# Performance work log

Measured on AMD Instinct MI355X. Metric: run time of the kernel, lower is better.

Reference implementation:

```python
import jax, jax.numpy as jnp
import numpy as np
import math

D_MODEL = 1024
N_HEADS = 16
D_HEAD = D_MODEL // N_HEADS
D_FF = 4096
BOTTLENECK = D_MODEL // 4  # 256
AB_HIDDEN = max(D_MODEL // 32, 8)  # 32
EPS = 1e-6


def rms_norm(x, w):
    rms = jnp.sqrt(jnp.mean(x * x, axis=-1, keepdims=True) + EPS)
    return x / rms * w


def rotate_half(x):
    x1, x2 = jnp.split(x, 2, axis=-1)
    return jnp.concatenate([-x2, x1], axis=-1)


def rope_tables(T, dim):
    inv_freq = 1.0 / (10000.0 ** (jnp.arange(0, dim, 2, dtype=jnp.float32) / dim))
    t = jnp.arange(T, dtype=jnp.float32)
    freqs = jnp.outer(t, inv_freq)            # [T, dim/2]
    emb = jnp.concatenate([freqs, freqs], -1)  # [T, dim]
    return jnp.cos(emb), jnp.sin(emb)


def setup_inputs() -> dict:
    key = jax.random.key(0)
    ks = jax.random.split(key, 12)
    B, T = 4, 2048
    s = lambda fan_in: 1.0 / math.sqrt(fan_in)
    x = jax.random.normal(ks[0], (B, T, D_MODEL), jnp.float32)
    mask = jnp.tril(jnp.ones((T, T), jnp.int32))  # causal 0/1 mask, mask==0 -> -inf
    return {
        "x": x,
        "mask": mask,
        "norm1_w": jnp.ones((D_MODEL,), jnp.float32),
        "Wq": jax.random.normal(ks[1], (D_MODEL, D_MODEL), jnp.float32) * s(D_MODEL),
        "Wk": jax.random.normal(ks[2], (D_MODEL, D_MODEL), jnp.float32) * s(D_MODEL),
        "Wv": jax.random.normal(ks[3], (D_MODEL, D_MODEL), jnp.float32) * s(D_MODEL),
        "Wo": jax.random.normal(ks[4], (D_MODEL, D_MODEL), jnp.float32) * s(D_MODEL),
        "norm2_w": jnp.ones((D_MODEL,), jnp.float32),
        "w1": jax.random.normal(ks[5], (D_FF, D_MODEL), jnp.float32) * s(D_MODEL),
        "w2": jax.random.normal(ks[6], (D_MODEL, D_FF), jnp.float32) * s(D_FF),
        "fc1": jax.random.normal(ks[7], (AB_HIDDEN, D_MODEL), jnp.float32) * s(D_MODEL),
        "fc2": jax.random.normal(ks[8], (2, AB_HIDDEN), jnp.float32) * s(AB_HIDDEN),
        "down": jax.random.normal(ks[9], (BOTTLENECK, D_MODEL), jnp.float32) * s(D_MODEL),
        "up": jax.random.normal(ks[10], (D_MODEL, BOTTLENECK), jnp.float32) * s(BOTTLENECK),
    }


def attention(x, mask, Wq, Wk, Wv, Wo):
    B, T, D = x.shape
    def split_heads(y):
        return y.reshape(B, T, N_HEADS, D_HEAD).transpose(0, 2, 1, 3)  # [B,H,T,Dh]
    q = split_heads(x @ Wq.T)
    k = split_heads(x @ Wk.T)
    v = split_heads(x @ Wv.T)
    cos, sin = rope_tables(T, D_HEAD)
    cos = cos[None, None]; sin = sin[None, None]
    q = q * cos + rotate_half(q) * sin
    k = k * cos + rotate_half(k) * sin
    scores = jnp.einsum("bhqd,bhkd->bhqk", q, k) / math.sqrt(D_HEAD)
    scores = jnp.where(mask[:T, :T] == 0, -jnp.inf, scores)
    attn = jax.nn.softmax(scores, axis=-1)
    out = jnp.einsum("bhqk,bhkd->bhqd", attn, v)
    out = out.transpose(0, 2, 1, 3).reshape(B, T, D)
    return out @ Wo.T


def reference(x, mask, norm1_w, Wq, Wk, Wv, Wo, norm2_w, w1, w2, fc1, fc2, down, up):
    # group='B': gated FFN + projection branch (dropout=0 / eval mode)
    x = x + attention(rms_norm(x, norm1_w), mask, Wq, Wk, Wv, Wo)
    normed = rms_norm(x, norm2_w)
    ffn_out = jax.nn.gelu(normed @ w1.T, approximate=False) @ w2.T
    # AttentionAlphaBetaLM: mean over tokens, tiny MLP -> (alpha, beta)
    g = normed.mean(axis=1)                      # [B, D]
    h = jax.nn.relu(g @ fc1.T)                   # [B, hidden]
    ab = h @ fc2.T                               # [B, 2]
    alpha = jax.nn.sigmoid(ab[:, 0])             # [B]
    beta = jax.nn.sigmoid(ab[:, 1])              # allow_negative_beta=False for group B
    proj_out = jax.nn.relu(normed @ down.T) @ up.T
    x = x + alpha[:, None, None] * ffn_out + beta[:, None, None] * proj_out
    return x
```

## Files before the change

kernel.cpp:

```cpp
#include <hip/hip_runtime.h>
#include <hip/hip_bf16.h>
#include <math.h>

typedef unsigned short u16;
typedef unsigned int   u32;

typedef __bf16 bf16x8_t __attribute__((ext_vector_type(8)));
typedef float  f32x4_t  __attribute__((ext_vector_type(4)));

__device__ float AB_dev[8];

__device__ inline float bf2f(u16 u) {
    u32 x = ((u32)u) << 16;
    return __builtin_bit_cast(float, x);
}
__device__ inline u16 f2bf(float f) {
    u32 x = __builtin_bit_cast(u32, f);
    return (u16)((x + 0x7fffu + ((x >> 16) & 1u)) >> 16);
}
__device__ inline u32 cvt_pk_bf16(float lo, float hi) {
    u32 r;
    asm("v_cvt_pk_bf16_f32 %0, %1, %2" : "=v"(r) : "v"(lo), "v"(hi));
    return r;
}
__device__ inline uint4 stage_pack_f32(const float* p) {
    float4 f0 = ((const float4*)p)[0];
    float4 f1 = ((const float4*)p)[1];
    u32 w0 = (u32)f2bf(f0.x) | ((u32)f2bf(f0.y) << 16);
    u32 w1 = (u32)f2bf(f0.z) | ((u32)f2bf(f0.w) << 16);
    u32 w2 = (u32)f2bf(f1.x) | ((u32)f2bf(f1.y) << 16);
    u32 w3 = (u32)f2bf(f1.z) | ((u32)f2bf(f1.w) << 16);
    return uint4{w0, w1, w2, w3};
}
#define GLD(gptr, lptr) __builtin_amdgcn_global_load_lds( \
    (const __attribute__((address_space(1))) void*)(gptr), \
    (__attribute__((address_space(3))) void*)(lptr), 16, 0, 0)

template <typename TIN>
__global__ __launch_bounds__(256) void rmsnorm_kernel(
    const TIN* __restrict__ x, const float* __restrict__ w, u16* __restrict__ out)
{
    const int row = blockIdx.x, tid = threadIdx.x;
    const size_t rb = (size_t)row * 1024;
    float val[4];
#pragma unroll
    for (int i = 0; i < 4; ++i) {
        size_t idx = rb + tid + i * 256;
        if constexpr (sizeof(TIN) == 4) val[i] = ((const float*)x)[idx];
        else                            val[i] = bf2f(((const u16*)x)[idx]);
    }
    float ss = val[0]*val[0] + val[1]*val[1] + val[2]*val[2] + val[3]*val[3];
#pragma unroll
    for (int off = 32; off >= 1; off >>= 1) ss += __shfl_xor(ss, off, 64);
    __shared__ float red[4];
    if ((tid & 63) == 0) red[tid >> 6] = ss;
    __syncthreads();
    float tot = red[0] + red[1] + red[2] + red[3];
    float inv = rsqrtf(tot * (1.0f / 1024.0f) + 1e-6f);
    u16* orow = out + rb;
#pragma unroll
    for (int i = 0; i < 4; ++i)
        orow[tid + i * 256] = f2bf(val[i] * inv * w[tid + i * 256]);
}

__global__ __launch_bounds__(256) void convm_kernel(
    const float* __restrict__ s0, const float* __restrict__ s1,
    const float* __restrict__ s2, const float* __restrict__ s3,
    u16* __restrict__ d0, u16* __restrict__ d1,
    u16* __restrict__ d2, u16* __restrict__ d3, int shift)
{
    int sel = blockIdx.x >> shift;
    int loc = blockIdx.x & ((1 << shift) - 1);
    const float* s = sel == 0 ? s0 : sel == 1 ? s1 : sel == 2 ? s2 : s3;
    u16*       d = sel == 0 ? d0 : sel == 1 ? d1 : sel == 2 ? d2 : d3;
    size_t i = ((size_t)loc * 256 + threadIdx.x) * 8;
    *(uint4*)(d + i) = stage_pack_f32(s + i);
}

enum { EPI_QKV = 0, EPI_ADDX_F32 = 1, EPI_GELU = 2, EPI_COMB0 = 3,
       EPI_COMBA = 4, EPI_RELU = 5, EPI_BSCALE = 6 };

__device__ inline void xcd_remap(int& bx, int& by) {
    int nwg = gridDim.x * gridDim.y;
    int bid = blockIdx.y * gridDim.x + blockIdx.x;
    int q8 = nwg >> 3;
    int swz = (bid & 7) * q8 + (bid >> 3);
    bx = swz % gridDim.x;
    by = swz / gridDim.x;
}

template <int EPI>
__global__ __launch_bounds__(256) void gemm128e(
    const u16* __restrict__ A, int sA, const u16* __restrict__ Wb, int sW,
    void* __restrict__ C, const float* __restrict__ Xf,
    const u16* __restrict__ Xh, int N, int K)
{
    __shared__ __align__(16) u16 As[2][128 * 32];
    __shared__ __align__(16) u16 Bs[2][128 * 32];
    const int tid  = threadIdx.x;
    const int wave = tid >> 6, lane = tid & 63;
    const int quad = lane >> 4, l16 = lane & 15;
    int bxx, byy;
    xcd_remap(bxx, byy);
    const int row0 = byy * 128, col0 = bxx * 128;
    const int wm = (wave >> 1) * 64, wn = (wave & 1) * 64;

    f32x4_t acc[4][4];
#pragma unroll
    for (int i = 0; i < 4; ++i)
#pragma unroll
        for (int j = 0; j < 4; ++j) { f32x4_t z = {0,0,0,0}; acc[i][j] = z; }

    const u16* Abase = A + (size_t)row0 * sA;
    const int id0 = tid, id1 = tid + 256;
    const size_t aoff0 = (size_t)(id0 >> 2) * sA + (id0 & 3) * 8;
    const size_t aoff1 = (size_t)(id1 >> 2) * sA + (id1 & 3) * 8;
    const size_t boff0 = (size_t)(col0 + (id0 >> 2)) * sW + (id0 & 3) * 8;
    const size_t boff1 = (size_t)(col0 + (id1 >> 2)) * sW + (id1 & 3) * 8;
    const size_t ld0 = (size_t)(wave * 64) * 8;
    const size_t ld1 = (size_t)(256 + wave * 64) * 8;

    for (int k0 = 0; k0 < K; k0 += 64) {
        __syncthreads();
        GLD(Abase + aoff0 + k0,      As[0] + ld0);
        GLD(Abase + aoff1 + k0,      As[0] + ld1);
        GLD(Abase + aoff0 + k0 + 32, As[1] + ld0);
        GLD(Abase + aoff1 + k0 + 32, As[1] + ld1);
        GLD(Wb + boff0 + k0,         Bs[0] + ld0);
        GLD(Wb + boff1 + k0,         Bs[0] + ld1);
        GLD(Wb + boff0 + k0 + 32,    Bs[1] + ld0);
        GLD(Wb + boff1 + k0 + 32,    Bs[1] + ld1);
        __syncthreads();

#pragma unroll
        for (int hh = 0; hh < 2; ++hh) {
            const bf16x8_t* As8 = (const bf16x8_t*)As[hh];
            const bf16x8_t* Bs8 = (const bf16x8_t*)Bs[hh];
            bf16x8_t af[4], bfr[4];
#pragma unroll
            for (int i = 0; i < 4; ++i) {
                af[i]  = As8[(wm + i * 16 + l16) * 4 + quad];
                bfr[i] = Bs8[(wn + i * 16 + l16) * 4 + quad];
            }
#pragma unroll
            for (int i = 0; i < 4; ++i)
#pragma unroll
                for (int j = 0; j < 4; ++j)
                    acc[i][j] = __builtin_amdgcn_mfma_f32_16x16x32_bf16(
                        af[i], bfr[j], acc[i][j], 0, 0, 0);
        }
    }

    float al = 0.0f;
    if (EPI == EPI_COMB0 || EPI == EPI_COMBA)
        al = AB_dev[byy >> 4];
#pragma unroll
    for (int i = 0; i < 4; ++i) {
        int mbase = row0 + wm + i * 16 + quad * 4;
#pragma unroll
        for (int j = 0; j < 4; ++j) {
            int n = col0 + wn + j * 16 + l16;
#pragma unroll
            for (int r = 0; r < 4; ++r) {
                float vv = acc[i][j][r];
                int row = mbase + r;
                if (EPI == EPI_QKV) {
                    int sel = col0 >> 10;
                    float sc = (sel == 0) ? 0.18033688011112042f : 1.0f;
                    ((u16*)C)[(size_t)sel * 8388608 + (size_t)row * 1024 + (n & 1023)]
                        = f2bf(vv * sc);
                } else if (EPI == EPI_ADDX_F32) {
                    size_t off = (size_t)row * N + n;
                    ((u16*)C)[off] = f2bf(vv + Xf[off]);
                } else if (EPI == EPI_GELU) {
                    size_t off = (size_t)row * N + n;
                    vv = 0.5f * vv * (1.0f + erff(vv * 0.70710678118654752f));
                    ((u16*)C)[off] = f2bf(vv);
                } else {
                    size_t off = (size_t)row * N + n;
                    float prev = ((float*)C)[off];
                    float add = (EPI == EPI_COMB0) ? bf2f(Xh[off]) : 0.0f;
                    ((float*)C)[off] = prev + add + al * vv;
                }
            }
        }
    }
}

template <int EPI>
__global__ __launch_bounds__(256) void gemm64b(
    const u16* __restrict__ A, int sA, const u16* __restrict__ Wb, int sW,
    void* __restrict__ C, int N, int K)
{
    __shared__ __align__(16) u16 As[2][128 * 32];
    __shared__ __align__(16) u16 Bs[2][64 * 32];
    const int tid  = threadIdx.x;
    const int wave = tid >> 6, lane = tid & 63;
    const int quad = lane >> 4, l16 = lane & 15;
    int bxx, byy;
    xcd_remap(bxx, byy);
    const int row0 = byy * 128, col0 = bxx * 64;
    const int wm = (wave >> 1) * 64, wn = (wave & 1) * 32;

    f32x4_t acc[4][2];
#pragma unroll
    for (int i = 0; i < 4; ++i)
#pragma unroll
        for (int j = 0; j < 2; ++j) { f32x4_t z = {0,0,0,0}; acc[i][j] = z; }

    const u16* Abase = A + (size_t)row0 * sA;
    const int id0 = tid, id1 = tid + 256;
    const size_t aoff0 = (size_t)(id0 >> 2) * sA + (id0 & 3) * 8;
    const size_t aoff1 = (size_t)(id1 >> 2) * sA + (id1 & 3) * 8;
    const size_t woff  = (size_t)(col0 + (tid >> 2)) * sW + (tid & 3) * 8;
    const size_t ld0 = (size_t)(wave * 64) * 8;
    const size_t ld1 = (size_t)(256 + wave * 64) * 8;

    for (int k0 = 0; k0 < K; k0 += 64) {
        __syncthreads();
        GLD(Abase + aoff0 + k0,      As[0] + ld0);
        GLD(Abase + aoff1 + k0,      As[0] + ld1);
        GLD(Abase + aoff0 + k0 + 32, As[1] + ld0);
        GLD(Abase + aoff1 + k0 + 32, As[1] + ld1);
        GLD(Wb + woff + k0,          Bs[0] + ld0);
        GLD(Wb + woff + k0 + 32,     Bs[1] + ld0);
        __syncthreads();

#pragma unroll
        for (int hh = 0; hh < 2; ++hh) {
            const bf16x8_t* As8 = (const bf16x8_t*)As[hh];
            const bf16x8_t* Bs8 = (const bf16x8_t*)Bs[hh];
            bf16x8_t af[4], bfr[2];
#pragma unroll
            for (int i = 0; i < 4; ++i) af[i]  = As8[(wm + i * 16 + l16) * 4 + quad];
#pragma unroll
            for (int j = 0; j < 2; ++j) bfr[j] = Bs8[(wn + j * 16 + l16) * 4 + quad];
#pragma unroll
            for (int i = 0; i < 4; ++i)
#pragma unroll
                for (int j = 0; j < 2; ++j)
                    acc[i][j] = __builtin_amdgcn_mfma_f32_16x16x32_bf16(
                        af[i], bfr[j], acc[i][j], 0, 0, 0);
        }
    }

#pragma unroll
    for (int i = 0; i < 4; ++i) {
        int mbase = row0 + wm + i * 16 + quad * 4;
#pragma unroll
        for (int j = 0; j < 2; ++j) {
            int n = col0 + wn + j * 16 + l16;
#pragma unroll
            for (int r = 0; r < 4; ++r) {
                float vv = acc[i][j][r];
                int row = mbase + r;
                size_t off = (size_t)row * N + n;
                if (EPI == EPI_RELU) {
                    ((u16*)C)[off] = f2bf(fmaxf(vv, 0.0f));
                } else {
                    ((float*)C)[off] = AB_dev[4 + (row >> 11)] * vv;
                }
            }
        }
    }
}

__global__ __launch_bounds__(256) void rope_kernel(u16* __restrict__ q, u16* __restrict__ k)
{
    int idx = blockIdx.x * 256 + threadIdx.x;
    int i = idx & 31;
    int h = (idx >> 5) & 15;
    int t = (idx >> 9) & 2047;
    int b = idx >> 20;
    float inv = __expf(-(float)i * (9.210340371976184f / 32.0f));
    float ang = (float)t * inv;
    float sn, cs;
    sincosf(ang, &sn, &cs);
    size_t o1 = ((size_t)(b * 2048 + t)) * 1024 + h * 64 + i;
    size_t o2 = o1 + 32;
    float q1 = bf2f(q[o1]), q2 = bf2f(q[o2]);
    q[o1] = f2bf(q1 * cs - q2 * sn);
    q[o2] = f2bf(q2 * cs + q1 * sn);
    float k1 = bf2f(k[o1]), k2 = bf2f(k[o2]);
    k[o1] = f2bf(k1 * cs - k2 * sn);
    k[o2] = f2bf(k2 * cs + k1 * sn);
}

#define TS 72

__global__ __launch_bounds__(256) void flash_kernel(
    const u16* __restrict__ q, const u16* __restrict__ k,
    const u16* __restrict__ v, u16* __restrict__ o)
{
    __shared__ __align__(16) u16 QP[128 * TS];
    __shared__ __align__(16) u16 KT[2][64 * 64];
    __shared__ __align__(16) u16 VT[64 * TS];

    const int tid  = threadIdx.x;
    const int wave = tid >> 6, lane = tid & 63;
    const int quad = lane >> 4, l16 = lane & 15;
    const int bx = blockIdx.x;
    const int p  = 15 - (bx >> 6);
    const int bh = bx & 63;
    const int h = bh & 15, b = bh >> 4;
    const int q0 = p * 128;
    const int qb0 = q0 + wave * 16;
    const int qb1 = q0 + 64 + wave * 16;
    const int last0 = qb0 + 15;
    const size_t bt_base = (size_t)(b * 2048) * 1024 + h * 64;

    const u16* kbase = k + bt_base;
    const u16* vbase = v + bt_base;
    const int psw = l16 & 7;

    uint4 vr[2];
#pragma unroll
    for (int it = 0; it < 2; ++it) {
        int id = it * 256 + tid;
        int row = id >> 3, c = id & 7;
        GLD(kbase + (size_t)row * 1024 + (c ^ (row & 7)) * 8,
            KT[0] + (size_t)(it * 256 + wave * 64) * 8);
        vr[it] = *(const uint4*)(vbase + (size_t)row * 1024 + c * 8);
    }
#pragma unroll
    for (int it = 0; it < 4; ++it) {
        int id = it * 256 + tid;
        int row = id >> 3, c8 = (id & 7) * 8;
        uint4 val = *(const uint4*)(q + bt_base + (size_t)(q0 + row) * 1024 + c8);
        *(uint4*)(QP + row * TS + c8) = val;
    }
    __syncthreads();

    bf16x8_t qf[2][2];
#pragma unroll
    for (int mi = 0; mi < 2; ++mi)
#pragma unroll
        for (int ks = 0; ks < 2; ++ks)
            qf[mi][ks] = *(const bf16x8_t*)(
                QP + (mi * 64 + wave * 16 + l16) * TS + ks * 32 + quad * 8);

#pragma unroll
    for (int it = 0; it < 2; ++it) {
        int id = it * 256 + tid;
        int row = id >> 3, c8 = (id & 7) * 8;
        const u16* vp = (const u16*)&vr[it];
        int sw = id & 7;
#pragma unroll
        for (int jj = 0; jj < 8; ++jj) {
            int j2 = (jj + sw) & 7;
            VT[(c8 + j2) * TS + row] = vp[j2];
        }
    }
    __syncthreads();

    float mst[2], lst[2];
    mst[0] = mst[1] = -3.0e38f;
    lst[0] = lst[1] = 0.f;
    f32x4_t oacc[2][4];
#pragma unroll
    for (int mi = 0; mi < 2; ++mi)
#pragma unroll
        for (int dj = 0; dj < 4; ++dj) { f32x4_t z = {0,0,0,0}; oacc[mi][dj] = z; }

    u16* Pl = (u16*)QP + wave * 2048;
    const int jmax = q0 + 128;
    int cur = 0;

    for (int j0 = 0; j0 < jmax; j0 += 64) {
        const bool more = (j0 + 64 < jmax);
        if (more) {
            const int jn = j0 + 64;
#pragma unroll
            for (int it = 0; it < 2; ++it) {
                int id = it * 256 + tid;
                int row = id >> 3, c = id & 7;
                GLD(kbase + (size_t)(jn + row) * 1024 + (c ^ (row & 7)) * 8,
                    KT[cur ^ 1] + (size_t)(it * 256 + wave * 64) * 8);
                vr[it] = *(const uint4*)(vbase + (size_t)(jn + row) * 1024 + c * 8);
            }
        }

        const bool a0 = (j0 <= last0);
        const u16* KTc = KT[cur];

        f32x4_t s[2][4];
#pragma unroll
        for (int mi = 0; mi < 2; ++mi)
#pragma unroll
            for (int nj = 0; nj < 4; ++nj) { f32x4_t z = {0,0,0,0}; s[mi][nj] = z; }
#pragma unroll
        for (int ks = 0; ks < 2; ++ks) {
            bf16x8_t kf2[4];
#pragma unroll
            for (int nj = 0; nj < 4; ++nj)
                kf2[nj] = *(const bf16x8_t*)(
                    KTc + (nj * 16 + l16) * 64 + (((ks * 4 + quad) ^ psw) * 8));
#pragma unroll
            for (int nj = 0; nj < 4; ++nj)
                s[1][nj] = __builtin_amdgcn_mfma_f32_16x16x32_bf16(
                    kf2[nj], qf[1][ks], s[1][nj], 0, 0, 0);
            if (a0) {
#pragma unroll
                for (int nj = 0; nj < 4; ++nj)
                    s[0][nj] = __builtin_amdgcn_mfma_f32_16x16x32_bf16(
                        kf2[nj], qf[0][ks], s[0][nj], 0, 0, 0);
            }
        }

        if (a0 && j0 + 63 > qb0) {
#pragma unroll
            for (int nj = 0; nj < 4; ++nj)
#pragma unroll
                for (int r = 0; r < 4; ++r) {
                    int key = j0 + nj * 16 + quad * 4 + r;
                    if (key > qb0 + l16) s[0][nj][r] = -1.0e30f;
                }
        }
        if (j0 + 63 > qb1) {
#pragma unroll
            for (int nj = 0; nj < 4; ++nj)
#pragma unroll
                for (int r = 0; r < 4; ++r) {
                    int key = j0 + nj * 16 + quad * 4 + r;
                    if (key > qb1 + l16) s[1][nj][r] = -1.0e30f;
                }
        }

#pragma unroll
        for (int mi = 0; mi < 2; ++mi) {
            if (mi == 0 && !a0) continue;
            float mx = s[mi][0][0];
#pragma unroll
            for (int nj = 0; nj < 4; ++nj)
#pragma unroll
                for (int r = 0; r < 4; ++r)
                    if (nj || r) mx = fmaxf(mx, s[mi][nj][r]);
            mx = fmaxf(mx, __shfl_xor(mx, 16, 64));
            mx = fmaxf(mx, __shfl_xor(mx, 32, 64));
            const bool skip = __all(mx - mst[mi] <= 8.0f);
            float mn, alpha = 1.0f;
            if (skip) {
                mn = mst[mi];
            } else {
                mn = fmaxf(mst[mi], mx);
                alpha = __builtin_amdgcn_exp2f(mst[mi] - mn);
                mst[mi] = mn;
            }
            float rs = 0.f;
            u16* prow = Pl + (mi * 16 + l16) * 64;
#pragma unroll
            for (int nj = 0; nj < 4; ++nj) {
                float p0 = __builtin_amdgcn_exp2f(s[mi][nj][0] - mn);
                float p1 = __builtin_amdgcn_exp2f(s[mi][nj][1] - mn);
                float p2 = __builtin_amdgcn_exp2f(s[mi][nj][2] - mn);
                float p3 = __builtin_amdgcn_exp2f(s[mi][nj][3] - mn);
                rs += (p0 + p1) + (p2 + p3);
                uint2 w;
                w.x = cvt_pk_bf16(p0, p1);
                w.y = cvt_pk_bf16(p2, p3);
                *(uint2*)(prow + (((nj * 2 + (quad >> 1)) ^ psw) * 8)
                               + (quad & 1) * 4) = w;
            }
            rs += __shfl_xor(rs, 16, 64);
            rs += __shfl_xor(rs, 32, 64);
            if (skip) {
                lst[mi] += rs;
            } else {
                lst[mi] = lst[mi] * alpha + rs;
#pragma unroll
                for (int r = 0; r < 4; ++r) {
                    float ar = __shfl(alpha, quad * 4 + r, 64);
#pragma unroll
                    for (int dj = 0; dj < 4; ++dj) oacc[mi][dj][r] *= ar;
                }
            }
        }

#pragma unroll
        for (int ks = 0; ks < 2; ++ks) {
            bf16x8_t vf2[4];
#pragma unroll
            for (int dj = 0; dj < 4; ++dj)
                vf2[dj] = *(const bf16x8_t*)(VT + (dj * 16 + l16) * TS + ks * 32 + quad * 8);
            bf16x8_t pf1 = *(const bf16x8_t*)(
                Pl + (16 + l16) * 64 + (((ks * 4 + quad) ^ psw) * 8));
#pragma unroll
            for (int dj = 0; dj < 4; ++dj)
                oacc[1][dj] = __builtin_amdgcn_mfma_f32_16x16x32_bf16(
                    pf1, vf2[dj], oacc[1][dj], 0, 0, 0);
            if (a0) {
                bf16x8_t pf0 = *(const bf16x8_t*)(
                    Pl + (l16) * 64 + (((ks * 4 + quad) ^ psw) * 8));
#pragma unroll
                for (int dj = 0; dj < 4; ++dj)
                    oacc[0][dj] = __builtin_amdgcn_mfma_f32_16x16x32_bf16(
                        pf0, vf2[dj], oacc[0][dj], 0, 0, 0);
            }
        }

        __syncthreads();
        if (more) {
#pragma unroll
            for (int it = 0; it < 2; ++it) {
                int id = it * 256 + tid;
                int row = id >> 3, c8 = (id & 7) * 8;
                const u16* vp = (const u16*)&vr[it];
                int sw = id & 7;
#pragma unroll
                for (int jj = 0; jj < 8; ++jj) {
                    int j2 = (jj + sw) & 7;
                    VT[(c8 + j2) * TS + row] = vp[j2];
                }
            }
        }
        __syncthreads();
        cur ^= 1;
    }

#pragma unroll
    for (int mi = 0; mi < 2; ++mi) {
        int gb = q0 + mi * 64 + wave * 16;
#pragma unroll
        for (int r = 0; r < 4; ++r) {
            float lr = __shfl(lst[mi], quad * 4 + r, 64);
            float invl = 1.0f / lr;
            size_t rowb = bt_base + (size_t)(gb + quad * 4 + r) * 1024;
#pragma unroll
            for (int dj = 0; dj < 4; ++dj)
                o[rowb + dj * 16 + l16] = f2bf(oacc[mi][dj][r] * invl);
        }
    }
}

__global__ __launch_bounds__(256) void mean_partial_kernel(
    const u16* __restrict__ normed, float* __restrict__ part)
{
    int blk = blockIdx.x;
    int b = blk >> 4, c = blk & 15;
    int tid = threadIdx.x;
    int d0 = tid * 4;
    float s0 = 0, s1 = 0, s2 = 0, s3 = 0;
    const u16* base = normed + ((size_t)b * 2048 + c * 128) * 1024 + d0;
    for (int t = 0; t < 128; ++t) {
        const uint2 uv = *(const uint2*)(base + (size_t)t * 1024);
        s0 += bf2f((u16)(uv.x & 0xffff));
        s1 += bf2f((u16)(uv.x >> 16));
        s2 += bf2f((u16)(uv.y & 0xffff));
        s3 += bf2f((u16)(uv.y >> 16));
    }
    float* o = part + (size_t)blk * 1024 + d0;
    o[0] = s0; o[1] = s1; o[2] = s2; o[3] = s3;
}

__global__ void ab_kernel(const float* __restrict__ part, const float* __restrict__ fc1,
                          const float* __restrict__ fc2)
{
    int b = blockIdx.x, tid = threadIdx.x;
    __shared__ float g[1024];
    __shared__ float h[32];
    for (int d = tid; d < 1024; d += 64) {
        float s = 0;
        for (int c = 0; c < 16; ++c) s += part[(size_t)(b * 16 + c) * 1024 + d];
        g[d] = s * (1.0f / 2048.0f);
    }
    __syncthreads();
    if (tid < 32) {
        float s = 0;
        for (int d = 0; d < 1024; ++d) s += g[d] * fc1[(size_t)tid * 1024 + d];
        h[tid] = fmaxf(s, 0.0f);
    }
    __syncthreads();
    if (tid < 2) {
        float s = 0;
        for (int j = 0; j < 32; ++j) s += h[j] * fc2[(size_t)tid * 32 + j];
        AB_dev[tid * 4 + b] = 1.0f / (1.0f + __expf(-s));
    }
}

__global__ __launch_bounds__(256) void sentinel_kernel(float* __restrict__ out, int n)
{
    int i = blockIdx.x * 256 + threadIdx.x;
    if (i < n) out[i] = 100.0f;
}

extern "C" void kernel_launch(void* const* d_in, const int* in_sizes, int n_in,
                              void* d_out, int out_size, void* d_ws, size_t ws_size,
                              hipStream_t stream)
{
    const float* x   = (const float*)d_in[0];
    const float* n1w = (const float*)d_in[2];
    const float* Wq  = (const float*)d_in[3];
    const float* Wk  = (const float*)d_in[4];
    const float* Wv  = (const float*)d_in[5];
    const float* Wo  = (const float*)d_in[6];
    const float* n2w = (const float*)d_in[7];
    const float* w1  = (const float*)d_in[8];
    const float* w2  = (const float*)d_in[9];
    const float* fc1 = (const float*)d_in[10];
    const float* fc2 = (const float*)d_in[11];
    const float* dwn = (const float*)d_in[12];
    const float* up  = (const float*)d_in[13];

    const size_t MB = 1024 * 1024;
    if (ws_size < 64 * MB) {
        sentinel_kernel<<<(out_size + 255) / 256, 256, 0, stream>>>((float*)d_out, out_size);
        return;
    }

    char* ws = (char*)d_ws;
    u16*   XN1  = (u16*)(ws);
    u16*   ATT  = (u16*)(ws);
    u16*   H1s  = (u16*)(ws);
    u16*   Q    = (u16*)(ws + 16 * MB);
    u16*   XNEW = (u16*)(ws + 16 * MB);
    u16*   K    = (u16*)(ws + 32 * MB);
    u16*   XN2  = (u16*)(ws + 32 * MB);
    u16*   V    = (u16*)(ws + 48 * MB);
    float* PART = (float*)(ws + 48 * MB);
    u16*   DWNB = (u16*)(ws + 48 * MB + 512 * 1024);
    u16*   W1B  = (u16*)(ws + 48 * MB);
    u16*   P1   = (u16*)(ws + 56 * MB);
    u16*   UPB  = (u16*)(ws + 60 * MB);
    u16*   W2B  = (u16*)(ws + 56 * MB);

    u16* WqkvB = (u16*)d_out;
    u16* WoB   = WqkvB + 3 * 1024 * 1024;

    dim3 blk(256);

    convm_kernel<<<2048, blk, 0, stream>>>(Wq, Wk, Wv, Wo,
        WqkvB, WqkvB + 1024 * 1024, WqkvB + 2 * 1024 * 1024, WoB, 9);
    rmsnorm_kernel<float><<<8192, blk, 0, stream>>>(x, n1w, XN1);
    gemm128e<EPI_QKV><<<dim3(24, 64), blk, 0, stream>>>(
        XN1, 1024, WqkvB, 1024, Q, nullptr, nullptr, 1024, 1024);
    rope_kernel<<<16384, blk, 0, stream>>>(Q, K);
    flash_kernel<<<1024, blk, 0, stream>>>(Q, K, V, ATT);
    gemm128e<EPI_ADDX_F32><<<dim3(8, 64), blk, 0, stream>>>(
        ATT, 1024, WoB, 1024, XNEW, x, nullptr, 1024, 1024);
    rmsnorm_kernel<u16><<<8192, blk, 0, stream>>>(XNEW, n2w, XN2);
    mean_partial_kernel<<<64, blk, 0, stream>>>(XN2, PART);
    ab_kernel<<<4, dim3(64), 0, stream>>>(PART, fc1, fc2);
    convm_kernel<<<256, blk, 0, stream>>>(dwn, up, nullptr, nullptr,
                                          DWNB, UPB, nullptr, nullptr, 7);
    gemm64b<EPI_RELU><<<dim3(4, 64), blk, 0, stream>>>(
        XN2, 1024, DWNB, 1024, P1, 256, 1024);
    convm_kernel<<<2048, blk, 0, stream>>>(w1, nullptr, nullptr, nullptr,
                                           W1B, nullptr, nullptr, nullptr, 11);
    gemm64b<EPI_BSCALE><<<dim3(16, 64), blk, 0, stream>>>(
        P1, 256, UPB, 256, d_out, 1024, 256);
    convm_kernel<<<2048, blk, 0, stream>>>(w2, nullptr, nullptr, nullptr,
                                           W2B, nullptr, nullptr, nullptr, 11);
    for (int s = 0; s < 4; ++s) {
        gemm128e<EPI_GELU><<<dim3(8, 64), blk, 0, stream>>>(
            XN2, 1024, W1B + (size_t)s * 1024 * 1024, 1024, H1s,
            nullptr, nullptr, 1024, 1024);
        if (s == 0)
            gemm128e<EPI_COMB0><<<dim3(8, 64), blk, 0, stream>>>(
                H1s, 1024, W2B + s * 1024, 4096, d_out,
                nullptr, XNEW, 1024, 1024);
        else
            gemm128e<EPI_COMBA><<<dim3(8, 64), blk, 0, stream>>>(
                H1s, 1024, W2B + s * 1024, 4096, d_out,
                nullptr, XNEW, 1024, 1024);
    }
}
```

Baseline: 719.5 us.

## Replace 128x128 GEMM with 256x256 swizzled, phase-pipelined 512-thread GEMM

Introduces a 256x256-tile GEMM with 8 waves, XOR-swizzled LDS layout, and a four-phase loop that interleaves next-tile global-to-LDS loads with MFMA quadrants under s_setprio and raw barriers. All 128-tile GEMM launches switch to it. The FFN chunk loop is regrouped so the middle two chunks share one wider GELU GEMM and one K=2048 down-projection. Larger tiles raise data reuse and cut LDS and global traffic per FLOP. The trade-off is that many launches now have 128 blocks, fewer than the CU count, and the 128 KB LDS footprint allows only one block per CU.

```diff
diff --git a/kernel.cpp b/kernel.cpp
--- a/kernel.cpp
+++ b/kernel.cpp
@@ -36,6 +36,8 @@
     (const __attribute__((address_space(1))) void*)(gptr), \
     (__attribute__((address_space(3))) void*)(lptr), 16, 0, 0)
 
+#define BARRIER() asm volatile("s_barrier" ::: "memory")
+
 template <typename TIN>
 __global__ __launch_bounds__(256) void rmsnorm_kernel(
     const TIN* __restrict__ x, const float* __restrict__ w, u16* __restrict__ out)
@@ -89,77 +91,145 @@
     by = swz / gridDim.x;
 }
 
+#define STAGE_A(ut, h) do { \
+    int rb_ = (h) * 128 + 16 * wave; \
+    _Pragma("unroll") \
+    for (int g_ = 0; g_ < 2; ++g_) \
+        GLD(A + (size_t)(row0 + rb_ + 8 * g_ + (lane >> 3)) * sA \
+              + (ut) * 64 + sw * 8, \
+            &As[(ut) & 1][(rb_ + 8 * g_) * 64]); \
+} while (0)
+#define STAGE_B(ut, h) do { \
+    int rb_ = (h) * 128 + 16 * wave; \
+    _Pragma("unroll") \
+    for (int g_ = 0; g_ < 2; ++g_) \
+        GLD(Wb + (size_t)(col0 + rb_ + 8 * g_ + (lane >> 3)) * sW \
+               + (ut) * 64 + sw * 8, \
+            &Bs[(ut) & 1][(rb_ + 8 * g_) * 64]); \
+} while (0)
+#define MFMA16(mq, nq) do { \
+    _Pragma("unroll") \
+    for (int i_ = 0; i_ < 4; ++i_) \
+        _Pragma("unroll") \
+        for (int j_ = 0; j_ < 2; ++j_) \
+            _Pragma("unroll") \
+            for (int kk_ = 0; kk_ < 2; ++kk_) \
+                acc[(mq) * 4 + i_][(nq) * 2 + j_] = \
+                    __builtin_amdgcn_mfma_f32_16x16x32_bf16( \
+                        afr[i_][kk_], bfr[j_][kk_], \
+                        acc[(mq) * 4 + i_][(nq) * 2 + j_], 0, 0, 0); \
+} while (0)
+
 template <int EPI>
-__global__ __launch_bounds__(256) void gemm128e(
+__global__ __launch_bounds__(512, 2) void gemm256(
     const u16* __restrict__ A, int sA, const u16* __restrict__ Wb, int sW,
     void* __restrict__ C, const float* __restrict__ Xf,
     const u16* __restrict__ Xh, int N, int K)
 {
-    __shared__ __align__(16) u16 As[2][128 * 32];
-    __shared__ __align__(16) u16 Bs[2][128 * 32];
+    __shared__ __align__(16) u16 As[2][256 * 64];
+    __shared__ __align__(16) u16 Bs[2][256 * 64];
     const int tid  = threadIdx.x;
     const int wave = tid >> 6, lane = tid & 63;
     const int quad = lane >> 4, l16 = lane & 15;
+    const int psw  = l16 & 7;
+    const int sw   = (lane & 7) ^ (lane >> 3);
+    const int wr = wave >> 2, wc = wave & 3;
     int bxx, byy;
     xcd_remap(bxx, byy);
-    const int row0 = byy * 128, col0 = bxx * 128;
-    const int wm = (wave >> 1) * 64, wn = (wave & 1) * 64;
-
-    f32x4_t acc[4][4];
-#pragma unroll
-    for (int i = 0; i < 4; ++i)
+    const int row0 = byy * 256, col0 = bxx * 256;
+
+    f32x4_t acc[8][4];
+#pragma unroll
+    for (int i = 0; i < 8; ++i)
 #pragma unroll
         for (int j = 0; j < 4; ++j) { f32x4_t z = {0,0,0,0}; acc[i][j] = z; }
 
-    const u16* Abase = A + (size_t)row0 * sA;
-    const int id0 = tid, id1 = tid + 256;
-    const size_t aoff0 = (size_t)(id0 >> 2) * sA + (id0 & 3) * 8;
-    const size_t aoff1 = (size_t)(id1 >> 2) * sA + (id1 & 3) * 8;
-    const size_t boff0 = (size_t)(col0 + (id0 >> 2)) * sW + (id0 & 3) * 8;
-    const size_t boff1 = (size_t)(col0 + (id1 >> 2)) * sW + (id1 & 3) * 8;
-    const size_t ld0 = (size_t)(wave * 64) * 8;
-    const size_t ld1 = (size_t)(256 + wave * 64) * 8;
-
-    for (int k0 = 0; k0 < K; k0 += 64) {
-        __syncthreads();
-        GLD(Abase + aoff0 + k0,      As[0] + ld0);
-        GLD(Abase + aoff1 + k0,      As[0] + ld1);
-        GLD(Abase + aoff0 + k0 + 32, As[1] + ld0);
-        GLD(Abase + aoff1 + k0 + 32, As[1] + ld1);
-        GLD(Wb + boff0 + k0,         Bs[0] + ld0);
-        GLD(Wb + boff1 + k0,         Bs[0] + ld1);
-        GLD(Wb + boff0 + k0 + 32,    Bs[1] + ld0);
-        GLD(Wb + boff1 + k0 + 32,    Bs[1] + ld1);
-        __syncthreads();
-
-#pragma unroll
-        for (int hh = 0; hh < 2; ++hh) {
-            const bf16x8_t* As8 = (const bf16x8_t*)As[hh];
-            const bf16x8_t* Bs8 = (const bf16x8_t*)Bs[hh];
-            bf16x8_t af[4], bfr[4];
-#pragma unroll
-            for (int i = 0; i < 4; ++i) {
-                af[i]  = As8[(wm + i * 16 + l16) * 4 + quad];
-                bfr[i] = Bs8[(wn + i * 16 + l16) * 4 + quad];
-            }
-#pragma unroll
-            for (int i = 0; i < 4; ++i)
-#pragma unroll
-                for (int j = 0; j < 4; ++j)
-                    acc[i][j] = __builtin_amdgcn_mfma_f32_16x16x32_bf16(
-                        af[i], bfr[j], acc[i][j], 0, 0, 0);
-        }
+    const int ntiles = K >> 6;
+
+    STAGE_A(0, 0); STAGE_B(0, 0); STAGE_A(0, 1); STAGE_B(0, 1);
+    STAGE_A(1, 0);
+    asm volatile("s_waitcnt vmcnt(2)" ::: "memory");
+    BARRIER();
+
+    for (int u = 0; u < ntiles; ++u) {
+        const u16* Ab = As[u & 1];
+        const u16* Bb = Bs[u & 1];
+        bf16x8_t afr[4][2], bfr[2][2];
+
+#pragma unroll
+        for (int i = 0; i < 4; ++i)
+#pragma unroll
+            for (int kk = 0; kk < 2; ++kk) {
+                int R = wr * 128 + i * 16 + l16;
+                afr[i][kk] = *(const bf16x8_t*)(Ab + R * 64 + (((kk * 4 + quad) ^ psw) * 8));
+            }
+#pragma unroll
+        for (int j = 0; j < 2; ++j)
+#pragma unroll
+            for (int kk = 0; kk < 2; ++kk) {
+                int R = wc * 64 + j * 16 + l16;
+                bfr[j][kk] = *(const bf16x8_t*)(Bb + R * 64 + (((kk * 4 + quad) ^ psw) * 8));
+            }
+        if (u + 1 < ntiles) STAGE_A(u + 1, 1);
+        BARRIER();
+        __builtin_amdgcn_s_setprio(1);
+        MFMA16(0, 0);
+        __builtin_amdgcn_s_setprio(0);
+        BARRIER();
+
+#pragma unroll
+        for (int j = 0; j < 2; ++j)
+#pragma unroll
+            for (int kk = 0; kk < 2; ++kk) {
+                int R = wc * 64 + 32 + j * 16 + l16;
+                bfr[j][kk] = *(const bf16x8_t*)(Bb + R * 64 + (((kk * 4 + quad) ^ psw) * 8));
+            }
+        if (u + 1 < ntiles) STAGE_B(u + 1, 0);
+        BARRIER();
+        __builtin_amdgcn_s_setprio(1);
+        MFMA16(0, 1);
+        __builtin_amdgcn_s_setprio(0);
+        BARRIER();
+
+#pragma unroll
+        for (int i = 0; i < 4; ++i)
+#pragma unroll
+            for (int kk = 0; kk < 2; ++kk) {
+                int R = wr * 128 + 64 + i * 16 + l16;
+                afr[i][kk] = *(const bf16x8_t*)(Ab + R * 64 + (((kk * 4 + quad) ^ psw) * 8));
+            }
+        if (u + 1 < ntiles) STAGE_B(u + 1, 1);
+        BARRIER();
+        __builtin_amdgcn_s_setprio(1);
+        MFMA16(1, 1);
+        __builtin_amdgcn_s_setprio(0);
+        BARRIER();
+
+#pragma unroll
+        for (int j = 0; j < 2; ++j)
+#pragma unroll
+            for (int kk = 0; kk < 2; ++kk) {
+                int R = wc * 64 + j * 16 + l16;
+                bfr[j][kk] = *(const bf16x8_t*)(Bb + R * 64 + (((kk * 4 + quad) ^ psw) * 8));
+            }
+        if (u + 2 < ntiles) STAGE_A(u + 2, 0);
+        asm volatile("s_waitcnt vmcnt(2)" ::: "memory");
+        BARRIER();
+        __builtin_amdgcn_s_setprio(1);
+        MFMA16(1, 0);
+        __builtin_amdgcn_s_setprio(0);
+        BARRIER();
     }
 
     float al = 0.0f;
     if (EPI == EPI_COMB0 || EPI == EPI_COMBA)
-        al = AB_dev[byy >> 4];
-#pragma unroll
-    for (int i = 0; i < 4; ++i) {
-        int mbase = row0 + wm + i * 16 + quad * 4;
+        al = AB_dev[byy >> 3];
+#pragma unroll
+    for (int i = 0; i < 8; ++i) {
+        int mbase = row0 + wr * 128 + i * 16 + quad * 4;
 #pragma unroll
         for (int j = 0; j < 4; ++j) {
-            int n = col0 + wn + j * 16 + l16;
+            int n = col0 + wc * 64 + j * 16 + l16;
 #pragma unroll
             for (int r = 0; r < 4; ++r) {
                 float vv = acc[i][j][r];
@@ -611,6 +681,7 @@
     u16*   XN1  = (u16*)(ws);
     u16*   ATT  = (u16*)(ws);
     u16*   H1s  = (u16*)(ws);
+    u16*   H1AB = (u16*)(ws);
     u16*   Q    = (u16*)(ws + 16 * MB);
     u16*   XNEW = (u16*)(ws + 16 * MB);
     u16*   K    = (u16*)(ws + 32 * MB);
@@ -627,15 +698,16 @@
     u16* WoB   = WqkvB + 3 * 1024 * 1024;
 
     dim3 blk(256);
+    dim3 blk5(512);
 
     convm_kernel<<<2048, blk, 0, stream>>>(Wq, Wk, Wv, Wo,
         WqkvB, WqkvB + 1024 * 1024, WqkvB + 2 * 1024 * 1024, WoB, 9);
     rmsnorm_kernel<float><<<8192, blk, 0, stream>>>(x, n1w, XN1);
-    gemm128e<EPI_QKV><<<dim3(24, 64), blk, 0, stream>>>(
+    gemm256<EPI_QKV><<<dim3(12, 32), blk5, 0, stream>>>(
         XN1, 1024, WqkvB, 1024, Q, nullptr, nullptr, 1024, 1024);
     rope_kernel<<<16384, blk, 0, stream>>>(Q, K);
     flash_kernel<<<1024, blk, 0, stream>>>(Q, K, V, ATT);
-    gemm128e<EPI_ADDX_F32><<<dim3(8, 64), blk, 0, stream>>>(
+    gemm256<EPI_ADDX_F32><<<dim3(4, 32), blk5, 0, stream>>>(
         ATT, 1024, WoB, 1024, XNEW, x, nullptr, 1024, 1024);
     rmsnorm_kernel<u16><<<8192, blk, 0, stream>>>(XNEW, n2w, XN2);
     mean_partial_kernel<<<64, blk, 0, stream>>>(XN2, PART);
@@ -650,17 +722,18 @@
         P1, 256, UPB, 256, d_out, 1024, 256);
     convm_kernel<<<2048, blk, 0, stream>>>(w2, nullptr, nullptr, nullptr,
                                            W2B, nullptr, nullptr, nullptr, 11);
-    for (int s = 0; s < 4; ++s) {
-        gemm128e<EPI_GELU><<<dim3(8, 64), blk, 0, stream>>>(
-            XN2, 1024, W1B + (size_t)s * 1024 * 1024, 1024, H1s,
-            nullptr, nullptr, 1024, 1024);
-        if (s == 0)
-            gemm128e<EPI_COMB0><<<dim3(8, 64), blk, 0, stream>>>(
-                H1s, 1024, W2B + s * 1024, 4096, d_out,
-                nullptr, XNEW, 1024, 1024);
-        else
-            gemm128e<EPI_COMBA><<<dim3(8, 64), blk, 0, stream>>>(
-                H1s, 1024, W2B + s * 1024, 4096, d_out,
-                nullptr, XNEW, 1024, 1024);
-    }
-}
+    gemm256<EPI_GELU><<<dim3(4, 32), blk5, 0, stream>>>(
+        XN2, 1024, W1B, 1024, H1s, nullptr, nullptr, 1024, 1024);
+    gemm256<EPI_COMB0><<<dim3(4, 32), blk5, 0, stream>>>(
+        H1s, 1024, W2B, 4096, d_out, nullptr, XNEW, 1024, 1024);
+    gemm256<EPI_GELU><<<dim3(8, 32), blk5, 0, stream>>>(
+        XN2, 1024, W1B + (size_t)1024 * 1024, 1024, H1AB, nullptr, nullptr,
+        2048, 1024);
+    gemm256<EPI_COMBA><<<dim3(4, 32), blk5, 0, stream>>>(
+        H1AB, 2048, W2B + 1024, 4096, d_out, nullptr, nullptr, 1024, 2048);
+    gemm256<EPI_GELU><<<dim3(4, 32), blk5, 0, stream>>>(
+        XN2, 1024, W1B + (size_t)3 * 1024 * 1024, 1024, H1s, nullptr, nullptr,
+        1024, 1024);
+    gemm256<EPI_COMBA><<<dim3(4, 32), blk5, 0, stream>>>(
+        H1s, 1024, W2B + 3072, 4096, d_out, nullptr, nullptr, 1024, 1024);
+}
```

Measured after the change: 812.1 us. +12.9%, slower.
